# Optimization experiments

Hardware: AMD Instinct MI355X
Metric: run time of the kernel (lower is better)

The kernel has to match this reference:

```python
import jax, jax.numpy as jnp
import numpy as np

H = 512

def _lstm_layer(x_tbd, W_ih, b, W_hh):
    # x_tbd: [T, B, D]; W_ih: [4H, D]; b: [4H]; W_hh: [4H, H]
    T, B, _ = x_tbd.shape
    # precompute input projections for all timesteps (same math, batched GEMM)
    xp = jnp.einsum('tbd,gd->tbg', x_tbd, W_ih) + b  # [T, B, 4H]

    def step(carry, xp_t):
        h, c = carry
        gates = xp_t + h @ W_hh.T  # [B, 4H]
        i, f, g, o = jnp.split(gates, 4, axis=-1)
        i = jax.nn.sigmoid(i)
        f = jax.nn.sigmoid(f)
        g = jnp.tanh(g)
        o = jax.nn.sigmoid(o)
        c_next = f * c + i * g
        h_next = o * jnp.tanh(c_next)
        return (h_next, c_next), h_next

    h0 = jnp.zeros((B, H), dtype=x_tbd.dtype)
    c0 = jnp.zeros((B, H), dtype=x_tbd.dtype)
    (h_n, c_n), hs = jax.lax.scan(step, (h0, c0), xp)
    return hs, h_n, c_n  # hs: [T, B, H]


def setup_inputs() -> dict:
    key = jax.random.key(0)
    ks = jax.random.split(key, 5)
    D = 256
    x = jax.random.normal(ks[0], (32, 1024, D), dtype=jnp.float32)
    s = 0.05
    W_ih0 = jax.random.normal(ks[1], (4 * H, D), dtype=jnp.float32) * s
    W_hh0 = jax.random.normal(ks[2], (4 * H, H), dtype=jnp.float32) * s
    W_ih1 = jax.random.normal(ks[3], (4 * H, H), dtype=jnp.float32) * s
    W_hh1 = jax.random.normal(ks[4], (4 * H, H), dtype=jnp.float32) * s
    # bias init: zeros, forget-gate slice [H:2H] = 1.0 (per _init_weights)
    b = jnp.zeros((4 * H,), dtype=jnp.float32).at[H:2 * H].set(1.0)
    return {"x": x, "W_ih0": W_ih0, "b0": b, "W_hh0": W_hh0,
            "W_ih1": W_ih1, "b1": b, "W_hh1": W_hh1}


def reference(x, W_ih0, b0, W_hh0, W_ih1, b1, W_hh1):
    # batch_first: [B, T, D] -> [T, B, D]
    x_tbd = jnp.transpose(x, (1, 0, 2))
    hs0, h0n, c0n = _lstm_layer(x_tbd, W_ih0, b0, W_hh0)
    hs1, h1n, c1n = _lstm_layer(hs0, W_ih1, b1, W_hh1)
    output = jnp.transpose(hs1, (1, 0, 2))  # [B, T, H]
    h_n = jnp.stack([h0n, h1n], axis=0)  # [num_layers, B, H]
    c_n = jnp.stack([c0n, c1n], axis=0)
    return output, h_n, c_n
```

## Files before the change

kernel.cpp:

```cpp
#include <hip/hip_runtime.h>


typedef __bf16 bf16x8 __attribute__((ext_vector_type(8)));
typedef float  f32x4  __attribute__((ext_vector_type(4)));
typedef float  f32x2  __attribute__((ext_vector_type(2)));
typedef unsigned long long u64;
typedef unsigned int u32;

#define MFMA16(a, b, c) __builtin_amdgcn_mfma_f32_16x16x32_bf16((a), (b), (c), 0, 0, 0)
#define SCOPE_AGENT __HIP_MEMORY_SCOPE_AGENT

__device__ __forceinline__ float fsigm(float x) { return 1.0f / (1.0f + __expf(-x)); }
__device__ __forceinline__ float ftanh(float x) {
    x = fminf(15.0f, fmaxf(-15.0f, x));
    float e = __expf(2.0f * x);
    return (e - 1.0f) / (e + 1.0f);
}

__device__ __forceinline__ bf16x8 frag_from(u64 lo, u64 hi) {
    union { u64 u[2]; bf16x8 v; } x;
    x.u[0] = lo; x.u[1] = hi;
    return x.v;
}

__device__ __forceinline__ void poll_pairs16(const u64* __restrict__ base, int tid,
                                             u32 ph, u64* hv) {
    u64 q0[16], q1[16];
    u32 bad;
    do {
#pragma unroll
        for (int i = 0; i < 16; i++) {
            int f = i * 256 + tid;
            q0[i] = __hip_atomic_load(base + 2 * f,     __ATOMIC_RELAXED, SCOPE_AGENT);
            q1[i] = __hip_atomic_load(base + 2 * f + 1, __ATOMIC_RELAXED, SCOPE_AGENT);
        }
        bad = 0;
#pragma unroll
        for (int i = 0; i < 16; i++)
            bad |= ((u32)(q0[i] >> 32) ^ ph) | ((u32)(q1[i] >> 32) ^ ph);
    } while (bad != 0);
#pragma unroll
    for (int i = 0; i < 16; i++) hv[i] = (q0[i] & 0xFFFFFFFFull) | (q1[i] << 32);
}

__global__ void pack_w3(const float* __restrict__ W0, const float* __restrict__ W1,
                        const float* __restrict__ W2, __bf16* __restrict__ O0,
                        __bf16* __restrict__ O1, __bf16* __restrict__ O2) {
    int gtid = blockIdx.x * 256 + threadIdx.x;
    int sel  = gtid >> 17;
    const float* W = (sel == 0) ? W0 : (sel == 1) ? W1 : W2;
    __bf16* WB     = (sel == 0) ? O0 : (sel == 1) ? O1 : O2;
    int tid  = gtid & 131071;
    int lane = tid & 63;
    int kk   = (tid >> 6) & 15;
    int v    = (tid >> 10) & 3;
    int w    = tid >> 12;
    int n    = v * 16 + (lane & 15);
    int grow = (n >> 4) * 512 + w * 16 + (n & 15);
    int k0   = kk * 32 + (lane >> 4) * 8;
    const float* src = W + (size_t)grow * 512 + k0;
    bf16x8 val;
#pragma unroll
    for (int e = 0; e < 8; e++) val[e] = (__bf16)src[e];
    *(bf16x8*)(WB + (size_t)tid * 8) = val;
}

__global__ __launch_bounds__(256, 2) void gemm_xp(const float* __restrict__ A,
                                                  const float* __restrict__ W,
                                                  __bf16* __restrict__ out, int K) {
    const int tid = threadIdx.x, lane = tid & 63, wv = tid >> 6;
    const int bm = blockIdx.x >> 4, bn = blockIdx.x & 15;
    const int m_base = bm * 128 + (wv & 1) * 64;
    const int n_base = bn * 128 + (wv >> 1) * 64;
    const int kq = (lane >> 4) * 8;
    const int rl = lane & 15;

    f32x4 acc[4][4];
#pragma unroll
    for (int i = 0; i < 4; i++)
#pragma unroll
        for (int j = 0; j < 4; j++) acc[i][j] = (f32x4){0.f, 0.f, 0.f, 0.f};

    const int nk = K >> 5;
    for (int kk = 0; kk < nk; kk++) {
        int k0 = kk * 32 + kq;
        bf16x8 af[4], bfr[4];
#pragma unroll
        for (int mt = 0; mt < 4; mt++) {
            int row = m_base + mt * 16 + rl;
            const float* ap = A + (size_t)((row & 31) * 1024 + (row >> 5)) * K + k0;
#pragma unroll
            for (int e = 0; e < 8; e++) af[mt][e] = (__bf16)ap[e];
        }
#pragma unroll
        for (int nt = 0; nt < 4; nt++) {
            int n = n_base + nt * 16 + rl;
            const float* wp = W + (size_t)n * K + k0;
#pragma unroll
            for (int e = 0; e < 8; e++) bfr[nt][e] = (__bf16)wp[e];
        }
#pragma unroll
        for (int mt = 0; mt < 4; mt++)
#pragma unroll
            for (int nt = 0; nt < 4; nt++)
                acc[mt][nt] = MFMA16(af[mt], bfr[nt], acc[mt][nt]);
    }

    const int rq = (lane >> 4) * 4;
#pragma unroll
    for (int mt = 0; mt < 4; mt++)
#pragma unroll
        for (int nt = 0; nt < 4; nt++)
#pragma unroll
            for (int r = 0; r < 4; r++) {
                int row = m_base + mt * 16 + rq + r;
                int col = n_base + nt * 16 + rl;
                out[(size_t)row * 2048 + col] = (__bf16)acc[mt][nt][r];
            }
}

__global__ __launch_bounds__(256, 1) void lstm_pipe3(
    const __bf16* __restrict__ xp0,
    const __bf16* __restrict__ WB0,
    const __bf16* __restrict__ WBw1,
    const __bf16* __restrict__ WBi1,
    const float* __restrict__ bias0,
    const float* __restrict__ bias1,
    u64* __restrict__ hbuf0,
    u64* __restrict__ hbuf1,
    __bf16* __restrict__ hs0s,
    __bf16* __restrict__ xp1r,
    float* __restrict__ out_f32,
    float* __restrict__ hn_out,
    float* __restrict__ cn_out,
    int* __restrict__ fL0,
    int* __restrict__ fX,
    int* __restrict__ fL1) {
    const int tid  = threadIdx.x;
    const int role = blockIdx.x >> 5;
    const int w    = blockIdx.x & 31;
    const int lane = tid & 63;
    const int wv   = tid >> 6;

    __shared__ __bf16 h_lds[32 * 516];
    __shared__ float  g_lds[32 * 68];

    bf16x8 wreg[16];
    {
        const __bf16* WB = (role == 0) ? WB0 : (role == 1) ? WBi1 : WBw1;
        const __bf16* wb = WB + (size_t)(w * 4 + wv) * 16 * 512 + lane * 8;
#pragma unroll
        for (int kk = 0; kk < 16; kk++) wreg[kk] = *(const bf16x8*)(wb + kk * 512);
    }

    const int b  = tid >> 3;
    const int jp = tid & 7;
    const int j0 = w * 16 + jp * 2;
    const int pi = b * 256 + w * 8 + jp;
    const int arow = lane & 15;
    const int kq8  = (lane >> 4) * 8;

    f32x2 bsv[4];
    if (role != 1) {
        const float* bias = (role == 0) ? bias0 : bias1;
#pragma unroll
        for (int g = 0; g < 4; g++) bsv[g] = *(const f32x2*)(bias + g * 512 + j0);
    }
    float cc0 = 0.f, cc1 = 0.f;

    u64* hbuf = (role == 0) ? hbuf0 : hbuf1;

    u32 xc[4] = {0, 0, 0, 0}, xn[4] = {0, 0, 0, 0};
    if (role == 0) {
#pragma unroll
        for (int g = 0; g < 4; g++)
            xc[g] = *(const u32*)(xp0 + (size_t)b * 2048 + g * 512 + j0);
    }

    for (int t = 0; t < 1024; t++) {
        u64 hv[16];
        u32 xpr[4];

        if (role == 0) {
            int tn = (t < 1023) ? t + 1 : 1023;
#pragma unroll
            for (int g = 0; g < 4; g++)
                xn[g] = *(const u32*)(xp0 + (size_t)(tn * 32 + b) * 2048 + g * 512 + j0);
            if (t > 0) {
                poll_pairs16(hbuf0 + (size_t)(t & 1) * 8192, tid, (u32)(t >> 1) + 1, hv);
            } else {
#pragma unroll
                for (int i = 0; i < 16; i++) hv[i] = 0;
            }
        } else if (role == 1) {
            if (tid < 32)
                while (__hip_atomic_load(&fL0[tid * 1024 + t], __ATOMIC_RELAXED,
                                         SCOPE_AGENT) == 0) {}
            else if (tid == 32 && t >= 4)
                while (__hip_atomic_load(&fL1[w * 1024 + t - 4], __ATOMIC_RELAXED,
                                         SCOPE_AGENT) == 0) {}
            asm volatile("" ::: "memory");
            __syncthreads();
            const u64* hg = (const u64*)(hs0s + (size_t)t * 16384);
#pragma unroll
            for (int i = 0; i < 16; i++)
                hv[i] = __hip_atomic_load(hg + i * 256 + tid, __ATOMIC_RELAXED, SCOPE_AGENT);
        } else {
            if (tid == 32)
                while (__hip_atomic_load(&fX[w * 1024 + t], __ATOMIC_RELAXED,
                                         SCOPE_AGENT) == 0) {}
            asm volatile("" ::: "memory");
            __syncthreads();
            const __bf16* xs = xp1r + (size_t)(t & 3) * 65536 + (size_t)b * 2048 + j0;
#pragma unroll
            for (int g = 0; g < 4; g++)
                xpr[g] = __hip_atomic_load((const u32*)(xs + g * 512),
                                           __ATOMIC_RELAXED, SCOPE_AGENT);
            if (t > 0) {
                poll_pairs16(hbuf1 + (size_t)(t & 1) * 8192, tid, (u32)(t >> 1) + 1, hv);
            } else {
#pragma unroll
                for (int i = 0; i < 16; i++) hv[i] = 0;
            }
        }

#pragma unroll
        for (int i = 0; i < 16; i++) {
            int f  = (i * 256 + tid) * 4;
            int br = f >> 9, col = f & 511;
            *(u64*)(h_lds + br * 516 + col) = hv[i];
        }
        if (role == 2)
            asm volatile("s_waitcnt vmcnt(0)" ::: "memory");
        __syncthreads();
        if (role == 2 && tid == 0)
            __hip_atomic_store(&fL1[w * 1024 + t], 1, __ATOMIC_RELAXED, SCOPE_AGENT);

        f32x4 acc0 = (f32x4){0.f, 0.f, 0.f, 0.f};
        f32x4 acc1 = (f32x4){0.f, 0.f, 0.f, 0.f};
#pragma unroll
        for (int kk = 0; kk < 16; kk++) {
            const __bf16* p0 = h_lds + arow * 516 + kq8 + kk * 32;
            const __bf16* p1 = p0 + 16 * 516;
            bf16x8 a0 = frag_from(*(const u64*)p0, *(const u64*)(p0 + 4));
            bf16x8 a1 = frag_from(*(const u64*)p1, *(const u64*)(p1 + 4));
            acc0 = MFMA16(a0, wreg[kk], acc0);
            acc1 = MFMA16(a1, wreg[kk], acc1);
        }
        {
            int col   = wv * 16 + (lane & 15);
            int rbase = (lane >> 4) * 4;
#pragma unroll
            for (int r = 0; r < 4; r++) {
                g_lds[(rbase + r) * 68 + col]      = acc0[r];
                g_lds[(16 + rbase + r) * 68 + col] = acc1[r];
            }
        }
        __syncthreads();

        if (role == 1) {
            const float* gl = g_lds + b * 68 + jp * 2;
            __bf16* xd = xp1r + (size_t)(t & 3) * 65536 + (size_t)b * 2048 + j0;
#pragma unroll
            for (int g = 0; g < 4; g++) {
                f32x2 gv = *(const f32x2*)(gl + g * 16);
                union { __bf16 v2[2]; u32 u; } pu;
                pu.v2[0] = (__bf16)gv[0]; pu.v2[1] = (__bf16)gv[1];
                __hip_atomic_store((u32*)(xd + g * 512), pu.u,
                                   __ATOMIC_RELAXED, SCOPE_AGENT);
            }
            asm volatile("s_waitcnt vmcnt(0)" ::: "memory");
            __syncthreads();
            if (tid == 0)
                __hip_atomic_store(&fX[w * 1024 + t], 1, __ATOMIC_RELAXED, SCOPE_AGENT);
        } else {
            float hf0, hf1;
            {
                u32 x0 = (role == 0) ? xc[0] : xpr[0];
                u32 x1 = (role == 0) ? xc[1] : xpr[1];
                u32 x2 = (role == 0) ? xc[2] : xpr[2];
                u32 x3 = (role == 0) ? xc[3] : xpr[3];
                union { u32 u; __bf16 v2[2]; } xi, xf, xg, xo;
                xi.u = x0; xf.u = x1; xg.u = x2; xo.u = x3;
                const float* gl = g_lds + b * 68 + jp * 2;
                f32x2 gi = *(const f32x2*)(gl);
                f32x2 gf = *(const f32x2*)(gl + 16);
                f32x2 gg = *(const f32x2*)(gl + 32);
                f32x2 go = *(const f32x2*)(gl + 48);

                float i0 = fsigm(gi[0] + (float)xi.v2[0] + bsv[0][0]);
                float f0 = fsigm(gf[0] + (float)xf.v2[0] + bsv[1][0]);
                float g0 = ftanh(gg[0] + (float)xg.v2[0] + bsv[2][0]);
                float o0 = fsigm(go[0] + (float)xo.v2[0] + bsv[3][0]);
                cc0 = f0 * cc0 + i0 * g0;
                hf0 = o0 * ftanh(cc0);

                float i1 = fsigm(gi[1] + (float)xi.v2[1] + bsv[0][1]);
                float f1 = fsigm(gf[1] + (float)xf.v2[1] + bsv[1][1]);
                float g1 = ftanh(gg[1] + (float)xg.v2[1] + bsv[2][1]);
                float o1 = fsigm(go[1] + (float)xo.v2[1] + bsv[3][1]);
                cc1 = f1 * cc1 + i1 * g1;
                hf1 = o1 * ftanh(cc1);
            }
            union { __bf16 v2[2]; u32 u; } hu;
            hu.v2[0] = (__bf16)hf0; hu.v2[1] = (__bf16)hf1;

            u64 hp = (u64)hu.u | ((u64)((u32)((t + 1) >> 1) + 1) << 32);
            __hip_atomic_store(hbuf + (size_t)((t + 1) & 1) * 8192 + pi, hp,
                               __ATOMIC_RELAXED, SCOPE_AGENT);

            if (role == 0) {
                __hip_atomic_store((u32*)(hs0s + ((size_t)t * 32 + b) * 512 + j0), hu.u,
                                   __ATOMIC_RELAXED, SCOPE_AGENT);
                asm volatile("s_waitcnt vmcnt(0)" ::: "memory");
                __syncthreads();
                if (tid == 0)
                    __hip_atomic_store(&fL0[w * 1024 + t], 1, __ATOMIC_RELAXED, SCOPE_AGENT);
            } else {
                *(f32x2*)(out_f32 + (size_t)b * 524288 + (size_t)t * 512 + j0) =
                    (f32x2){hf0, hf1};
            }
            if (t == 1023) {
                int li = (role == 0) ? 0 : 1;
                *(f32x2*)(hn_out + (size_t)li * 16384 + (size_t)b * 512 + j0) =
                    (f32x2){hf0, hf1};
                *(f32x2*)(cn_out + (size_t)li * 16384 + (size_t)b * 512 + j0) =
                    (f32x2){cc0, cc1};
            }
#pragma unroll
            for (int g = 0; g < 4; g++) xc[g] = xn[g];
        }
    }
}

extern "C" void kernel_launch(void* const* d_in, const int* in_sizes, int n_in,
                              void* d_out, int out_size, void* d_ws, size_t ws_size,
                              hipStream_t stream) {
    (void)in_sizes; (void)n_in; (void)out_size; (void)ws_size;
    const float* x    = (const float*)d_in[0];
    const float* Wih0 = (const float*)d_in[1];
    const float* b0   = (const float*)d_in[2];
    const float* Whh0 = (const float*)d_in[3];
    const float* Wih1 = (const float*)d_in[4];
    const float* b1   = (const float*)d_in[5];
    const float* Whh1 = (const float*)d_in[6];
    float* dout = (float*)d_out;

    char* wsb = (char*)d_ws;
    int*    fL0   = (int*)wsb;
    int*    fX    = (int*)(wsb + (128 << 10));
    int*    fL1   = (int*)(wsb + (256 << 10));
    u64*    hbuf0 = (u64*)(wsb + (384 << 10));
    u64*    hbuf1 = (u64*)(wsb + (512 << 10));
    __bf16* WB0   = (__bf16*)(wsb + (640 << 10));
    __bf16* WBw1  = (__bf16*)(wsb + (640 << 10) + (2 << 20));
    __bf16* WBi1  = (__bf16*)(wsb + (640 << 10) + (4 << 20));
    __bf16* xp1r  = (__bf16*)(wsb + (640 << 10) + (6 << 20));
    __bf16* hs0s  = (__bf16*)(wsb + (8 << 20));
    __bf16* xpb   = (__bf16*)(wsb + (40 << 20));

    (void)hipMemsetAsync(wsb, 0, 640 << 10, stream);

    pack_w3<<<dim3(1536), dim3(256), 0, stream>>>(Whh0, Whh1, Wih1, WB0, WBw1, WBi1);

    gemm_xp<<<dim3(4096), dim3(256), 0, stream>>>(x, Wih0, xpb, 256);

    lstm_pipe3<<<dim3(96), dim3(256), 0, stream>>>(
        xpb, WB0, WBw1, WBi1, b0, b1, hbuf0, hbuf1, hs0s, xp1r,
        dout, dout + 16777216, dout + 16777216 + 32768, fL0, fX, fL1);
}
```

Measured before the change: 4.030 ms.

## Merge layer-1 input projection into recurrent blocks, use 8-deep tagged ring

Replaces the three-role 96-block pipeline with two roles in 64 blocks. Layer-1 blocks now hold both W_ih1 and W_hh1 in registers and compute the input projection themselves. They read layer-0 h from an 8-slot ring of tagged u64 entries, and the W_ih1 MFMAs run before polling for their own previous h, which hides that wait. Per-timestep flag arrays and the separate projection role go away; a progress counter lets layer 0 stall when it gets 8 steps ahead. The cost is twice the register footprint for weights in layer-1 blocks and more serial MFMA work on the layer-1 critical path.

```diff
diff --git a/kernel.cpp b/kernel.cpp
--- a/kernel.cpp
+++ b/kernel.cpp
@@ -9,6 +9,7 @@
 
 #define MFMA16(a, b, c) __builtin_amdgcn_mfma_f32_16x16x32_bf16((a), (b), (c), 0, 0, 0)
 #define SCOPE_AGENT __HIP_MEMORY_SCOPE_AGENT
+#define AL64(p) __hip_atomic_load((p), __ATOMIC_RELAXED, SCOPE_AGENT)
 
 __device__ __forceinline__ float fsigm(float x) { return 1.0f / (1.0f + __expf(-x)); }
 __device__ __forceinline__ float ftanh(float x) {
@@ -31,8 +32,8 @@
 #pragma unroll
         for (int i = 0; i < 16; i++) {
             int f = i * 256 + tid;
-            q0[i] = __hip_atomic_load(base + 2 * f,     __ATOMIC_RELAXED, SCOPE_AGENT);
-            q1[i] = __hip_atomic_load(base + 2 * f + 1, __ATOMIC_RELAXED, SCOPE_AGENT);
+            q0[i] = AL64(base + 2 * f);
+            q1[i] = AL64(base + 2 * f + 1);
         }
         bad = 0;
 #pragma unroll
@@ -119,7 +120,7 @@
             }
 }
 
-__global__ __launch_bounds__(256, 1) void lstm_pipe3(
+__global__ __launch_bounds__(256, 1) void lstm_pipe2(
     const __bf16* __restrict__ xp0,
     const __bf16* __restrict__ WB0,
     const __bf16* __restrict__ WBw1,
@@ -128,30 +129,19 @@
     const float* __restrict__ bias1,
     u64* __restrict__ hbuf0,
     u64* __restrict__ hbuf1,
-    __bf16* __restrict__ hs0s,
-    __bf16* __restrict__ xp1r,
+    u64* __restrict__ ring,
+    u32* __restrict__ prog1,
     float* __restrict__ out_f32,
     float* __restrict__ hn_out,
-    float* __restrict__ cn_out,
-    int* __restrict__ fL0,
-    int* __restrict__ fX,
-    int* __restrict__ fL1) {
+    float* __restrict__ cn_out) {
     const int tid  = threadIdx.x;
     const int role = blockIdx.x >> 5;
     const int w    = blockIdx.x & 31;
     const int lane = tid & 63;
     const int wv   = tid >> 6;
 
-    __shared__ __bf16 h_lds[32 * 516];
+    __shared__ __bf16 lds_h[32 * 516];
     __shared__ float  g_lds[32 * 68];
-
-    bf16x8 wreg[16];
-    {
-        const __bf16* WB = (role == 0) ? WB0 : (role == 1) ? WBi1 : WBw1;
-        const __bf16* wb = WB + (size_t)(w * 4 + wv) * 16 * 512 + lane * 8;
-#pragma unroll
-        for (int kk = 0; kk < 16; kk++) wreg[kk] = *(const bf16x8*)(wb + kk * 512);
-    }
 
     const int b  = tid >> 3;
     const int jp = tid & 7;
@@ -161,127 +151,82 @@
     const int kq8  = (lane >> 4) * 8;
 
     f32x2 bsv[4];
-    if (role != 1) {
+    {
         const float* bias = (role == 0) ? bias0 : bias1;
 #pragma unroll
         for (int g = 0; g < 4; g++) bsv[g] = *(const f32x2*)(bias + g * 512 + j0);
     }
     float cc0 = 0.f, cc1 = 0.f;
 
-    u64* hbuf = (role == 0) ? hbuf0 : hbuf1;
-
-    u32 xc[4] = {0, 0, 0, 0}, xn[4] = {0, 0, 0, 0};
     if (role == 0) {
+        bf16x8 wreg[16];
+        {
+            const __bf16* wb = WB0 + (size_t)(w * 4 + wv) * 16 * 512 + lane * 8;
+#pragma unroll
+            for (int kk = 0; kk < 16; kk++) wreg[kk] = *(const bf16x8*)(wb + kk * 512);
+        }
+        u32 xc[4], xn[4];
 #pragma unroll
         for (int g = 0; g < 4; g++)
             xc[g] = *(const u32*)(xp0 + (size_t)b * 2048 + g * 512 + j0);
-    }
-
-    for (int t = 0; t < 1024; t++) {
-        u64 hv[16];
-        u32 xpr[4];
-
-        if (role == 0) {
-            int tn = (t < 1023) ? t + 1 : 1023;
-#pragma unroll
-            for (int g = 0; g < 4; g++)
-                xn[g] = *(const u32*)(xp0 + (size_t)(tn * 32 + b) * 2048 + g * 512 + j0);
+
+        for (int t = 0; t < 1024; t++) {
+            u32 pv = 0;
+            if (tid < 32 && t >= 8)
+                pv = __hip_atomic_load(&prog1[tid], __ATOMIC_RELAXED, SCOPE_AGENT);
+
+            u64 hv[16];
             if (t > 0) {
                 poll_pairs16(hbuf0 + (size_t)(t & 1) * 8192, tid, (u32)(t >> 1) + 1, hv);
             } else {
 #pragma unroll
                 for (int i = 0; i < 16; i++) hv[i] = 0;
             }
-        } else if (role == 1) {
-            if (tid < 32)
-                while (__hip_atomic_load(&fL0[tid * 1024 + t], __ATOMIC_RELAXED,
-                                         SCOPE_AGENT) == 0) {}
-            else if (tid == 32 && t >= 4)
-                while (__hip_atomic_load(&fL1[w * 1024 + t - 4], __ATOMIC_RELAXED,
-                                         SCOPE_AGENT) == 0) {}
-            asm volatile("" ::: "memory");
-            __syncthreads();
-            const u64* hg = (const u64*)(hs0s + (size_t)t * 16384);
-#pragma unroll
-            for (int i = 0; i < 16; i++)
-                hv[i] = __hip_atomic_load(hg + i * 256 + tid, __ATOMIC_RELAXED, SCOPE_AGENT);
-        } else {
-            if (tid == 32)
-                while (__hip_atomic_load(&fX[w * 1024 + t], __ATOMIC_RELAXED,
-                                         SCOPE_AGENT) == 0) {}
-            asm volatile("" ::: "memory");
-            __syncthreads();
-            const __bf16* xs = xp1r + (size_t)(t & 3) * 65536 + (size_t)b * 2048 + j0;
-#pragma unroll
-            for (int g = 0; g < 4; g++)
-                xpr[g] = __hip_atomic_load((const u32*)(xs + g * 512),
-                                           __ATOMIC_RELAXED, SCOPE_AGENT);
-            if (t > 0) {
-                poll_pairs16(hbuf1 + (size_t)(t & 1) * 8192, tid, (u32)(t >> 1) + 1, hv);
-            } else {
-#pragma unroll
-                for (int i = 0; i < 16; i++) hv[i] = 0;
-            }
-        }
-
-#pragma unroll
-        for (int i = 0; i < 16; i++) {
-            int f  = (i * 256 + tid) * 4;
-            int br = f >> 9, col = f & 511;
-            *(u64*)(h_lds + br * 516 + col) = hv[i];
-        }
-        if (role == 2)
-            asm volatile("s_waitcnt vmcnt(0)" ::: "memory");
-        __syncthreads();
-        if (role == 2 && tid == 0)
-            __hip_atomic_store(&fL1[w * 1024 + t], 1, __ATOMIC_RELAXED, SCOPE_AGENT);
-
-        f32x4 acc0 = (f32x4){0.f, 0.f, 0.f, 0.f};
-        f32x4 acc1 = (f32x4){0.f, 0.f, 0.f, 0.f};
-#pragma unroll
-        for (int kk = 0; kk < 16; kk++) {
-            const __bf16* p0 = h_lds + arow * 516 + kq8 + kk * 32;
-            const __bf16* p1 = p0 + 16 * 516;
-            bf16x8 a0 = frag_from(*(const u64*)p0, *(const u64*)(p0 + 4));
-            bf16x8 a1 = frag_from(*(const u64*)p1, *(const u64*)(p1 + 4));
-            acc0 = MFMA16(a0, wreg[kk], acc0);
-            acc1 = MFMA16(a1, wreg[kk], acc1);
-        }
-        {
-            int col   = wv * 16 + (lane & 15);
-            int rbase = (lane >> 4) * 4;
-#pragma unroll
-            for (int r = 0; r < 4; r++) {
-                g_lds[(rbase + r) * 68 + col]      = acc0[r];
-                g_lds[(16 + rbase + r) * 68 + col] = acc1[r];
-            }
-        }
-        __syncthreads();
-
-        if (role == 1) {
-            const float* gl = g_lds + b * 68 + jp * 2;
-            __bf16* xd = xp1r + (size_t)(t & 3) * 65536 + (size_t)b * 2048 + j0;
-#pragma unroll
-            for (int g = 0; g < 4; g++) {
-                f32x2 gv = *(const f32x2*)(gl + g * 16);
-                union { __bf16 v2[2]; u32 u; } pu;
-                pu.v2[0] = (__bf16)gv[0]; pu.v2[1] = (__bf16)gv[1];
-                __hip_atomic_store((u32*)(xd + g * 512), pu.u,
-                                   __ATOMIC_RELAXED, SCOPE_AGENT);
-            }
-            asm volatile("s_waitcnt vmcnt(0)" ::: "memory");
-            __syncthreads();
-            if (tid == 0)
-                __hip_atomic_store(&fX[w * 1024 + t], 1, __ATOMIC_RELAXED, SCOPE_AGENT);
-        } else {
+            if (tid < 32 && t >= 8)
+                while ((int)pv < t - 7)
+                    pv = __hip_atomic_load(&prog1[tid], __ATOMIC_RELAXED, SCOPE_AGENT);
+
+            {
+                int tn = (t < 1023) ? t + 1 : 1023;
+#pragma unroll
+                for (int g = 0; g < 4; g++)
+                    xn[g] = *(const u32*)(xp0 + (size_t)(tn * 32 + b) * 2048 + g * 512 + j0);
+            }
+
+#pragma unroll
+            for (int i = 0; i < 16; i++) {
+                int f  = (i * 256 + tid) * 4;
+                int br = f >> 9, col = f & 511;
+                *(u64*)(lds_h + br * 516 + col) = hv[i];
+            }
+            __syncthreads();
+
+            f32x4 acc0 = (f32x4){0.f, 0.f, 0.f, 0.f};
+            f32x4 acc1 = (f32x4){0.f, 0.f, 0.f, 0.f};
+#pragma unroll
+            for (int kk = 0; kk < 16; kk++) {
+                const __bf16* p0 = lds_h + arow * 516 + kq8 + kk * 32;
+                const __bf16* p1 = p0 + 16 * 516;
+                bf16x8 a0 = frag_from(*(const u64*)p0, *(const u64*)(p0 + 4));
+                bf16x8 a1 = frag_from(*(const u64*)p1, *(const u64*)(p1 + 4));
+                acc0 = MFMA16(a0, wreg[kk], acc0);
+                acc1 = MFMA16(a1, wreg[kk], acc1);
+            }
+            {
+                int col   = wv * 16 + (lane & 15);
+                int rbase = (lane >> 4) * 4;
+#pragma unroll
+                for (int r = 0; r < 4; r++) {
+                    g_lds[(rbase + r) * 68 + col]      = acc0[r];
+                    g_lds[(16 + rbase + r) * 68 + col] = acc1[r];
+                }
+            }
+            __syncthreads();
+
             float hf0, hf1;
             {
-                u32 x0 = (role == 0) ? xc[0] : xpr[0];
-                u32 x1 = (role == 0) ? xc[1] : xpr[1];
-                u32 x2 = (role == 0) ? xc[2] : xpr[2];
-                u32 x3 = (role == 0) ? xc[3] : xpr[3];
                 union { u32 u; __bf16 v2[2]; } xi, xf, xg, xo;
-                xi.u = x0; xf.u = x1; xg.u = x2; xo.u = x3;
+                xi.u = xc[0]; xf.u = xc[1]; xg.u = xc[2]; xo.u = xc[3];
                 const float* gl = g_lds + b * 68 + jp * 2;
                 f32x2 gi = *(const f32x2*)(gl);
                 f32x2 gf = *(const f32x2*)(gl + 16);
@@ -305,30 +250,161 @@
             union { __bf16 v2[2]; u32 u; } hu;
             hu.v2[0] = (__bf16)hf0; hu.v2[1] = (__bf16)hf1;
 
-            u64 hp = (u64)hu.u | ((u64)((u32)((t + 1) >> 1) + 1) << 32);
-            __hip_atomic_store(hbuf + (size_t)((t + 1) & 1) * 8192 + pi, hp,
+            u64 hp_rec = (u64)hu.u | ((u64)((u32)((t + 1) >> 1) + 1) << 32);
+            __hip_atomic_store(hbuf0 + (size_t)((t + 1) & 1) * 8192 + pi, hp_rec,
                                __ATOMIC_RELAXED, SCOPE_AGENT);
-
-            if (role == 0) {
-                __hip_atomic_store((u32*)(hs0s + ((size_t)t * 32 + b) * 512 + j0), hu.u,
-                                   __ATOMIC_RELAXED, SCOPE_AGENT);
-                asm volatile("s_waitcnt vmcnt(0)" ::: "memory");
-                __syncthreads();
-                if (tid == 0)
-                    __hip_atomic_store(&fL0[w * 1024 + t], 1, __ATOMIC_RELAXED, SCOPE_AGENT);
+            u64 hp_ring = (u64)hu.u | ((u64)(u32)(t + 1) << 32);
+            __hip_atomic_store(ring + (size_t)(t & 7) * 8192 + pi, hp_ring,
+                               __ATOMIC_RELAXED, SCOPE_AGENT);
+
+            if (t == 1023) {
+                *(f32x2*)(hn_out + (size_t)b * 512 + j0) = (f32x2){hf0, hf1};
+                *(f32x2*)(cn_out + (size_t)b * 512 + j0) = (f32x2){cc0, cc1};
+            }
+#pragma unroll
+            for (int g = 0; g < 4; g++) xc[g] = xn[g];
+        }
+    } else {
+        bf16x8 wregA[16], wregB[16];
+        {
+            const __bf16* wa = WBi1 + (size_t)(w * 4 + wv) * 16 * 512 + lane * 8;
+            const __bf16* wb = WBw1 + (size_t)(w * 4 + wv) * 16 * 512 + lane * 8;
+#pragma unroll
+            for (int kk = 0; kk < 16; kk++) {
+                wregA[kk] = *(const bf16x8*)(wa + kk * 512);
+                wregB[kk] = *(const bf16x8*)(wb + kk * 512);
+            }
+        }
+
+        for (int t = 0; t < 1024; t++) {
+            u64 qa[16], qb[16];
+            if (t > 0) {
+                const u64* hb = hbuf1 + (size_t)(t & 1) * 8192;
+#pragma unroll
+                for (int i = 0; i < 16; i++) {
+                    int f = i * 256 + tid;
+                    qa[i] = AL64(hb + 2 * f);
+                    qb[i] = AL64(hb + 2 * f + 1);
+                }
+            }
+
+            u64 hvx[16];
+            poll_pairs16(ring + (size_t)(t & 7) * 8192, tid, (u32)(t + 1), hvx);
+
+#pragma unroll
+            for (int i = 0; i < 16; i++) {
+                int f  = (i * 256 + tid) * 4;
+                int br = f >> 9, col = f & 511;
+                *(u64*)(lds_h + br * 516 + col) = hvx[i];
+            }
+            __syncthreads();
+
+            f32x4 acc0 = (f32x4){0.f, 0.f, 0.f, 0.f};
+            f32x4 acc1 = (f32x4){0.f, 0.f, 0.f, 0.f};
+#pragma unroll
+            for (int kk = 0; kk < 16; kk++) {
+                const __bf16* p0 = lds_h + arow * 516 + kq8 + kk * 32;
+                const __bf16* p1 = p0 + 16 * 516;
+                bf16x8 a0 = frag_from(*(const u64*)p0, *(const u64*)(p0 + 4));
+                bf16x8 a1 = frag_from(*(const u64*)p1, *(const u64*)(p1 + 4));
+                acc0 = MFMA16(a0, wregA[kk], acc0);
+                acc1 = MFMA16(a1, wregA[kk], acc1);
+            }
+            __syncthreads();
+
+            u64 hv[16];
+            if (t > 0) {
+                const u64* hb = hbuf1 + (size_t)(t & 1) * 8192;
+                u32 ph = (u32)(t >> 1) + 1;
+                u32 bad = 0;
+#pragma unroll
+                for (int i = 0; i < 16; i++)
+                    bad |= ((u32)(qa[i] >> 32) ^ ph) | ((u32)(qb[i] >> 32) ^ ph);
+                while (bad != 0) {
+#pragma unroll
+                    for (int i = 0; i < 16; i++) {
+                        int f = i * 256 + tid;
+                        qa[i] = AL64(hb + 2 * f);
+                        qb[i] = AL64(hb + 2 * f + 1);
+                    }
+                    bad = 0;
+#pragma unroll
+                    for (int i = 0; i < 16; i++)
+                        bad |= ((u32)(qa[i] >> 32) ^ ph) | ((u32)(qb[i] >> 32) ^ ph);
+                }
+#pragma unroll
+                for (int i = 0; i < 16; i++)
+                    hv[i] = (qa[i] & 0xFFFFFFFFull) | (qb[i] << 32);
             } else {
-                *(f32x2*)(out_f32 + (size_t)b * 524288 + (size_t)t * 512 + j0) =
-                    (f32x2){hf0, hf1};
-            }
+#pragma unroll
+                for (int i = 0; i < 16; i++) hv[i] = 0;
+            }
+
+#pragma unroll
+            for (int i = 0; i < 16; i++) {
+                int f  = (i * 256 + tid) * 4;
+                int br = f >> 9, col = f & 511;
+                *(u64*)(lds_h + br * 516 + col) = hv[i];
+            }
+            __syncthreads();
+
+#pragma unroll
+            for (int kk = 0; kk < 16; kk++) {
+                const __bf16* p0 = lds_h + arow * 516 + kq8 + kk * 32;
+                const __bf16* p1 = p0 + 16 * 516;
+                bf16x8 a0 = frag_from(*(const u64*)p0, *(const u64*)(p0 + 4));
+                bf16x8 a1 = frag_from(*(const u64*)p1, *(const u64*)(p1 + 4));
+                acc0 = MFMA16(a0, wregB[kk], acc0);
+                acc1 = MFMA16(a1, wregB[kk], acc1);
+            }
+            {
+                int col   = wv * 16 + (lane & 15);
+                int rbase = (lane >> 4) * 4;
+#pragma unroll
+                for (int r = 0; r < 4; r++) {
+                    g_lds[(rbase + r) * 68 + col]      = acc0[r];
+                    g_lds[(16 + rbase + r) * 68 + col] = acc1[r];
+                }
+            }
+            __syncthreads();
+
+            float hf0, hf1;
+            {
+                const float* gl = g_lds + b * 68 + jp * 2;
+                f32x2 gi = *(const f32x2*)(gl);
+                f32x2 gf = *(const f32x2*)(gl + 16);
+                f32x2 gg = *(const f32x2*)(gl + 32);
+                f32x2 go = *(const f32x2*)(gl + 48);
+
+                float i0 = fsigm(gi[0] + bsv[0][0]);
+                float f0 = fsigm(gf[0] + bsv[1][0]);
+                float g0 = ftanh(gg[0] + bsv[2][0]);
+                float o0 = fsigm(go[0] + bsv[3][0]);
+                cc0 = f0 * cc0 + i0 * g0;
+                hf0 = o0 * ftanh(cc0);
+
+                float i1 = fsigm(gi[1] + bsv[0][1]);
+                float f1 = fsigm(gf[1] + bsv[1][1]);
+                float g1 = ftanh(gg[1] + bsv[2][1]);
+                float o1 = fsigm(go[1] + bsv[3][1]);
+                cc1 = f1 * cc1 + i1 * g1;
+                hf1 = o1 * ftanh(cc1);
+            }
+            union { __bf16 v2[2]; u32 u; } hu;
+            hu.v2[0] = (__bf16)hf0; hu.v2[1] = (__bf16)hf1;
+
+            u64 hp_rec = (u64)hu.u | ((u64)((u32)((t + 1) >> 1) + 1) << 32);
+            __hip_atomic_store(hbuf1 + (size_t)((t + 1) & 1) * 8192 + pi, hp_rec,
+                               __ATOMIC_RELAXED, SCOPE_AGENT);
+            *(f32x2*)(out_f32 + (size_t)b * 524288 + (size_t)t * 512 + j0) =
+                (f32x2){hf0, hf1};
+            if (tid == 0)
+                __hip_atomic_store(&prog1[w], (u32)(t + 1), __ATOMIC_RELAXED, SCOPE_AGENT);
+
             if (t == 1023) {
-                int li = (role == 0) ? 0 : 1;
-                *(f32x2*)(hn_out + (size_t)li * 16384 + (size_t)b * 512 + j0) =
-                    (f32x2){hf0, hf1};
-                *(f32x2*)(cn_out + (size_t)li * 16384 + (size_t)b * 512 + j0) =
-                    (f32x2){cc0, cc1};
-            }
-#pragma unroll
-            for (int g = 0; g < 4; g++) xc[g] = xn[g];
+                *(f32x2*)(hn_out + 16384 + (size_t)b * 512 + j0) = (f32x2){hf0, hf1};
+                *(f32x2*)(cn_out + 16384 + (size_t)b * 512 + j0) = (f32x2){cc0, cc1};
+            }
         }
     }
 }
@@ -347,25 +423,22 @@
     float* dout = (float*)d_out;
 
     char* wsb = (char*)d_ws;
-    int*    fL0   = (int*)wsb;
-    int*    fX    = (int*)(wsb + (128 << 10));
-    int*    fL1   = (int*)(wsb + (256 << 10));
-    u64*    hbuf0 = (u64*)(wsb + (384 << 10));
-    u64*    hbuf1 = (u64*)(wsb + (512 << 10));
-    __bf16* WB0   = (__bf16*)(wsb + (640 << 10));
-    __bf16* WBw1  = (__bf16*)(wsb + (640 << 10) + (2 << 20));
-    __bf16* WBi1  = (__bf16*)(wsb + (640 << 10) + (4 << 20));
-    __bf16* xp1r  = (__bf16*)(wsb + (640 << 10) + (6 << 20));
-    __bf16* hs0s  = (__bf16*)(wsb + (8 << 20));
-    __bf16* xpb   = (__bf16*)(wsb + (40 << 20));
-
-    (void)hipMemsetAsync(wsb, 0, 640 << 10, stream);
+    u32*    prog1 = (u32*)wsb;
+    u64*    hbuf0 = (u64*)(wsb + (4 << 10));
+    u64*    hbuf1 = (u64*)(wsb + (4 << 10) + (128 << 10));
+    u64*    ring  = (u64*)(wsb + (4 << 10) + (256 << 10));
+    __bf16* WB0   = (__bf16*)(wsb + (1 << 20));
+    __bf16* WBw1  = (__bf16*)(wsb + (3 << 20));
+    __bf16* WBi1  = (__bf16*)(wsb + (5 << 20));
+    __bf16* xpb   = (__bf16*)(wsb + (8 << 20));
+
+    (void)hipMemsetAsync(wsb, 0, 772 << 10, stream);
 
     pack_w3<<<dim3(1536), dim3(256), 0, stream>>>(Whh0, Whh1, Wih1, WB0, WBw1, WBi1);
 
     gemm_xp<<<dim3(4096), dim3(256), 0, stream>>>(x, Wih0, xpb, 256);
 
-    lstm_pipe3<<<dim3(96), dim3(256), 0, stream>>>(
-        xpb, WB0, WBw1, WBi1, b0, b1, hbuf0, hbuf1, hs0s, xp1r,
-        dout, dout + 16777216, dout + 16777216 + 32768, fL0, fX, fL1);
-}
+    lstm_pipe2<<<dim3(64), dim3(256), 0, stream>>>(
+        xpb, WB0, WBw1, WBi1, b0, b1, hbuf0, hbuf1, ring, prog1,
+        dout, dout + 16777216, dout + 16777216 + 32768);
+}
```

Measured after the change: 8.081 ms. 101% more time.
